# Kernel tuning notes

Measured on AMD Instinct MI355X. Metric: run time of the kernel, lower is better.

The kernel has to match this reference:

```python
import jax, jax.numpy as jnp
import numpy as np

N = 100000      # nodes
E = 1600000     # edges (avg degree 16)
D_IN, H, D_OUT = 128, 64, 40


def setup_inputs() -> dict:
    key = jax.random.key(0)
    k = jax.random.split(key, 6)
    x = jax.random.normal(k[0], (N, D_IN), dtype=jnp.float32)
    edge_index = jax.random.randint(k[1], (2, E), 0, N, dtype=jnp.int32)
    W1 = jax.random.normal(k[2], (D_IN, H), dtype=jnp.float32) / np.sqrt(D_IN)
    b1 = jnp.zeros((H,), dtype=jnp.float32)
    W2 = jax.random.normal(k[3], (H, D_OUT), dtype=jnp.float32) / np.sqrt(H)
    b2 = jnp.zeros((D_OUT,), dtype=jnp.float32)
    return {"x": x, "edge_index": edge_index, "W1": W1, "b1": b1, "W2": W2, "b2": b2}


def _gcn_conv(h, src, dst, dinv, W, b):
    # PyG GCNConv: linear transform, then D^-1/2 (A+I) D^-1/2 aggregation, then bias.
    h = h @ W                                   # [N, F]
    w = dinv[src] * dinv[dst]                   # [E] symmetric norm edge weights
    msg = h[src] * w[:, None]                   # [E, F] gather + scale
    agg = jax.ops.segment_sum(msg, dst, num_segments=N)  # scatter-add to dst
    agg = agg + h * (dinv * dinv)[:, None]      # self-loop contribution deg^-1 * h
    return agg + b


def reference(x, edge_index, W1, b1, W2, b2):
    src, dst = edge_index[0], edge_index[1]
    # degree with self-loops (in-degree at dst, source_to_target flow)
    deg = 1.0 + jax.ops.segment_sum(jnp.ones((E,), dtype=x.dtype), dst, num_segments=N)
    dinv = jax.lax.rsqrt(deg)
    # dropout (p=0.6) is identity in eval mode
    h = jax.nn.relu(_gcn_conv(x, src, dst, dinv, W1, b1))
    out = _gcn_conv(h, src, dst, dinv, W2, b2)
    return jax.nn.log_softmax(out, axis=1)
```

## Files before the change

### kernel.cpp

```cpp
#include <hip/hip_runtime.h>
#include <math.h>

#define D_IN  128
#define H_DIM 64
#define D_OUT 40
#define BW_SHIFT 9
#define BW_NODES 512
#define BINA_CHUNK 4096
#define BUCKET_CAP 9216

typedef unsigned int uint32;

__device__ __forceinline__ unsigned short f2bf(float v) {
    uint32 b = __float_as_uint(v);
    b += 0x7fffu + ((b >> 16) & 1u);
    return (unsigned short)(b >> 16);
}
__device__ __forceinline__ float bf2f(unsigned short u) {
    return __uint_as_float(((uint32)u) << 16);
}

__global__ void cursor_init_kernel(int* __restrict__ gcursor, int NBUCK) {
    int i = blockIdx.x * 256 + threadIdx.x;
    if (i < NBUCK) gcursor[i] = i * BUCKET_CAP;
}

__global__ __launch_bounds__(256) void binA_scatter_kernel(const int* __restrict__ src,
                                                           const int* __restrict__ dst,
                                                           int* __restrict__ gcursor,
                                                           uint32* __restrict__ binned,
                                                           int E, int NBUCK) {
    __shared__ int cnt[1024];
    __shared__ int lbase[1024];
    int t = threadIdx.x;
    for (int i = t; i < NBUCK; i += 256) cnt[i] = 0;
    __syncthreads();
    int e0 = blockIdx.x * BINA_CHUNK;
    int e1 = min(e0 + BINA_CHUNK, E);
    for (int e = e0 + t; e < e1; e += 256)
        atomicAdd(&cnt[dst[e] >> BW_SHIFT], 1);
    __syncthreads();
    for (int i = t; i < NBUCK; i += 256) {
        int c = cnt[i];
        lbase[i] = c ? atomicAdd(&gcursor[i], c) : 0;
        cnt[i] = 0;
    }
    __syncthreads();
    for (int e = e0 + t; e < e1; e += 256) {
        int d = dst[e];
        int bk = d >> BW_SHIFT;
        int p = lbase[bk] + atomicAdd(&cnt[bk], 1);
        binned[p] = (((uint32)(d & (BW_NODES - 1))) << 23) | (uint32)src[e];
    }
}

__global__ __launch_bounds__(256) void phaseB_kernel(uint32* __restrict__ binned,
                                                     const int* __restrict__ gcur_end,
                                                     int* __restrict__ rows,
                                                     float* __restrict__ dinv,
                                                     int N) {
    __shared__ uint32 sedge[BUCKET_CAP];
    __shared__ int deg[BW_NODES];
    __shared__ int sa[BW_NODES], sb[BW_NODES];
    __shared__ int cur[BW_NODES];
    int b = blockIdx.x;
    int node0 = b << BW_SHIFT;
    int nn = min(BW_NODES, N - node0);
    int base = b * BUCKET_CAP;
    int cnt = gcur_end[b] - base;
    int t = threadIdx.x;
    deg[t] = 0; deg[t + 256] = 0;
    __syncthreads();
    for (int e = t; e < cnt; e += 256) {
        uint32 v = binned[base + e];
        sedge[e] = v;
        atomicAdd(&deg[v >> 23], 1);
    }
    __syncthreads();
    for (int i = t; i < nn; i += 256)
        dinv[node0 + i] = rsqrtf(1.0f + (float)deg[i]);
    sa[t] = deg[t]; sa[t + 256] = deg[t + 256];
    __syncthreads();
    int* pa = sa; int* pb = sb;
    for (int off = 1; off < BW_NODES; off <<= 1) {
        for (int i = t; i < BW_NODES; i += 256)
            pb[i] = pa[i] + ((i >= off) ? pa[i - off] : 0);
        __syncthreads();
        int* tmp = pa; pa = pb; pb = tmp;
    }
    for (int i = t; i < BW_NODES; i += 256)
        cur[i] = (i ? pa[i - 1] : 0);
    __syncthreads();
    int* rb = rows + b * 513;
    for (int i = t; i < nn; i += 256)
        rb[i] = base + cur[i];
    if (t == 0) rb[nn] = base + cnt;
    __syncthreads();
    for (int e = t; e < cnt; e += 256) {
        uint32 v = sedge[e];
        int doff = v >> 23;
        int p = base + atomicAdd(&cur[doff], 1);
        binned[p] = v & 0x7FFFFFu;
    }
}

__global__ __launch_bounds__(256) void gemm1_tn4(const float* __restrict__ x,
                                                 const float* __restrict__ W1,
                                                 const float* __restrict__ dinv,
                                                 unsigned short* __restrict__ h1s, int N) {
    __shared__ float sW[D_IN * H_DIM];
    int t = threadIdx.x;
    for (int i = t; i < D_IN * H_DIM / 4; i += 256)
        reinterpret_cast<float4*>(sW)[i] = reinterpret_cast<const float4*>(W1)[i];
    __syncthreads();

    int n = blockIdx.x * 64 + (t >> 2);
    if (n >= N) return;
    int c0 = (t & 3) * 16;
    const float4* xr = reinterpret_cast<const float4*>(x + (size_t)n * D_IN);

    float acc[16] = {};
    for (int k0 = 0; k0 < D_IN / 4; ++k0) {
        float4 xv = xr[k0];
        #pragma unroll
        for (int kk = 0; kk < 4; ++kk) {
            float xk = (kk == 0) ? xv.x : (kk == 1) ? xv.y : (kk == 2) ? xv.z : xv.w;
            const float* wrow = &sW[(4 * k0 + kk) * H_DIM + c0];
            #pragma unroll
            for (int c = 0; c < 4; ++c) {
                float4 wv = *reinterpret_cast<const float4*>(wrow + 4 * c);
                acc[4 * c + 0] += xk * wv.x;
                acc[4 * c + 1] += xk * wv.y;
                acc[4 * c + 2] += xk * wv.z;
                acc[4 * c + 3] += xk * wv.w;
            }
        }
    }
    float di = dinv[n];
    unsigned short* orow = h1s + (size_t)n * H_DIM + c0;
    #pragma unroll
    for (int c = 0; c < 4; ++c) {
        ushort4 u;
        u.x = f2bf(acc[4 * c + 0] * di);
        u.y = f2bf(acc[4 * c + 1] * di);
        u.z = f2bf(acc[4 * c + 2] * di);
        u.w = f2bf(acc[4 * c + 3] * di);
        *reinterpret_cast<ushort4*>(orow + 4 * c) = u;
    }
}

__global__ __launch_bounds__(256) void agg1_v3(const int* __restrict__ rows,
                                               const int* __restrict__ csr,
                                               const unsigned short* __restrict__ h1s,
                                               const float* __restrict__ dinv,
                                               const float* __restrict__ b1,
                                               float* __restrict__ z, int N) {
    int node = blockIdx.x * 4 + (threadIdx.x >> 6);
    if (node >= N) return;
    int lane = threadIdx.x & 63;
    int e  = lane >> 4;
    int fl = (lane & 15) * 4;
    int ridx = node + (node >> BW_SHIFT);
    int s0 = __builtin_amdgcn_readfirstlane(rows[ridx]);
    int s1 = __builtin_amdgcn_readfirstlane(rows[ridx + 1]);

    float4 acc = make_float4(0.f, 0.f, 0.f, 0.f);
    for (int base = s0; base < s1; base += 64) {
        int cnt = min(64, s1 - base);
        int myc = (lane < cnt) ? csr[base + lane] : 0;
        int j = 0;
        for (; j + 8 <= cnt; j += 8) {
            uint32 sa = (uint32)__shfl(myc, j + e);
            uint32 sb = (uint32)__shfl(myc, j + 4 + e);
            ushort4 ha = *reinterpret_cast<const ushort4*>(h1s + (size_t)(sa * H_DIM + fl));
            ushort4 hb = *reinterpret_cast<const ushort4*>(h1s + (size_t)(sb * H_DIM + fl));
            acc.x += bf2f(ha.x) + bf2f(hb.x);
            acc.y += bf2f(ha.y) + bf2f(hb.y);
            acc.z += bf2f(ha.z) + bf2f(hb.z);
            acc.w += bf2f(ha.w) + bf2f(hb.w);
        }
        for (; j < cnt; j += 4) {
            int idx = j + e;
            uint32 sa = (uint32)__shfl(myc, min(idx, cnt - 1));
            if (idx < cnt) {
                ushort4 hv = *reinterpret_cast<const ushort4*>(h1s + (size_t)(sa * H_DIM + fl));
                acc.x += bf2f(hv.x); acc.y += bf2f(hv.y);
                acc.z += bf2f(hv.z); acc.w += bf2f(hv.w);
            }
        }
    }
    acc.x += __shfl_xor(acc.x, 16); acc.y += __shfl_xor(acc.y, 16);
    acc.z += __shfl_xor(acc.z, 16); acc.w += __shfl_xor(acc.w, 16);
    acc.x += __shfl_xor(acc.x, 32); acc.y += __shfl_xor(acc.y, 32);
    acc.z += __shfl_xor(acc.z, 32); acc.w += __shfl_xor(acc.w, 32);

    if (e == 0) {
        ushort4 sv = *reinterpret_cast<const ushort4*>(h1s + (size_t)node * H_DIM + fl);
        float4 bv = *reinterpret_cast<const float4*>(b1 + fl);
        float di = dinv[node];
        float4 o;
        o.x = fmaxf(0.f, di * (acc.x + bf2f(sv.x)) + bv.x);
        o.y = fmaxf(0.f, di * (acc.y + bf2f(sv.y)) + bv.y);
        o.z = fmaxf(0.f, di * (acc.z + bf2f(sv.z)) + bv.z);
        o.w = fmaxf(0.f, di * (acc.w + bf2f(sv.w)) + bv.w);
        *reinterpret_cast<float4*>(z + (size_t)node * H_DIM + fl) = o;
    }
}

__global__ __launch_bounds__(256) void gemm2_tn2(const float* __restrict__ z,
                                                 const float* __restrict__ W2,
                                                 const float* __restrict__ dinv,
                                                 unsigned short* __restrict__ h2s, int N) {
    __shared__ float sW[H_DIM * D_OUT];
    int t = threadIdx.x;
    for (int i = t; i < H_DIM * D_OUT / 4; i += 256)
        reinterpret_cast<float4*>(sW)[i] = reinterpret_cast<const float4*>(W2)[i];
    __syncthreads();

    int n = blockIdx.x * 128 + (t >> 1);
    if (n >= N) return;
    int c0 = (t & 1) * 20;
    const float4* zr = reinterpret_cast<const float4*>(z + (size_t)n * H_DIM);

    float acc[20] = {};
    for (int k0 = 0; k0 < H_DIM / 4; ++k0) {
        float4 zv = zr[k0];
        #pragma unroll
        for (int kk = 0; kk < 4; ++kk) {
            float zk = (kk == 0) ? zv.x : (kk == 1) ? zv.y : (kk == 2) ? zv.z : zv.w;
            const float* wrow = &sW[(4 * k0 + kk) * D_OUT + c0];
            #pragma unroll
            for (int c = 0; c < 5; ++c) {
                float4 wv = *reinterpret_cast<const float4*>(wrow + 4 * c);
                acc[4 * c + 0] += zk * wv.x;
                acc[4 * c + 1] += zk * wv.y;
                acc[4 * c + 2] += zk * wv.z;
                acc[4 * c + 3] += zk * wv.w;
            }
        }
    }
    float di = dinv[n];
    unsigned short* orow = h2s + (size_t)n * D_OUT + c0;
    #pragma unroll
    for (int c = 0; c < 5; ++c) {
        ushort4 u;
        u.x = f2bf(acc[4 * c + 0] * di);
        u.y = f2bf(acc[4 * c + 1] * di);
        u.z = f2bf(acc[4 * c + 2] * di);
        u.w = f2bf(acc[4 * c + 3] * di);
        *reinterpret_cast<ushort4*>(orow + 4 * c) = u;
    }
}

__global__ __launch_bounds__(256) void agg2_v4(const int* __restrict__ rows,
                                               const int* __restrict__ csr,
                                               const unsigned short* __restrict__ h2s,
                                               const float* __restrict__ dinv,
                                               const float* __restrict__ b2,
                                               float* __restrict__ out, int N) {
    int node = blockIdx.x * 4 + (threadIdx.x >> 6);
    if (node >= N) return;
    int lane = threadIdx.x & 63;
    int g   = lane / 10;
    int f10 = lane - g * 10;
    int fl  = f10 * 4;
    bool gact = g < 6;
    int ridx = node + (node >> BW_SHIFT);
    int s0 = __builtin_amdgcn_readfirstlane(rows[ridx]);
    int s1 = __builtin_amdgcn_readfirstlane(rows[ridx + 1]);

    float4 acc = make_float4(0.f, 0.f, 0.f, 0.f);
    for (int base = s0; base < s1; base += 64) {
        int cnt = min(64, s1 - base);
        int myc = (lane < cnt) ? csr[base + lane] : 0;
        int j = 0;
        for (; j + 12 <= cnt; j += 12) {
            uint32 sa = (uint32)__shfl(myc, min(j + g, 63));
            uint32 sb = (uint32)__shfl(myc, min(j + 6 + g, 63));
            if (gact) {
                ushort4 ha = *reinterpret_cast<const ushort4*>(h2s + (size_t)(sa * D_OUT + fl));
                ushort4 hb = *reinterpret_cast<const ushort4*>(h2s + (size_t)(sb * D_OUT + fl));
                acc.x += bf2f(ha.x) + bf2f(hb.x);
                acc.y += bf2f(ha.y) + bf2f(hb.y);
                acc.z += bf2f(ha.z) + bf2f(hb.z);
                acc.w += bf2f(ha.w) + bf2f(hb.w);
            }
        }
        for (; j < cnt; j += 6) {
            int idx = j + g;
            uint32 sa = (uint32)__shfl(myc, min(idx, cnt - 1));
            if (gact && idx < cnt) {
                ushort4 hv = *reinterpret_cast<const ushort4*>(h2s + (size_t)(sa * D_OUT + fl));
                acc.x += bf2f(hv.x); acc.y += bf2f(hv.y);
                acc.z += bf2f(hv.z); acc.w += bf2f(hv.w);
            }
        }
    }
    acc.x += __shfl(acc.x, min(lane + 30, 63));
    acc.y += __shfl(acc.y, min(lane + 30, 63));
    acc.z += __shfl(acc.z, min(lane + 30, 63));
    acc.w += __shfl(acc.w, min(lane + 30, 63));
    acc.x += __shfl(acc.x, min(lane + 10, 63)) + __shfl(acc.x, min(lane + 20, 63));
    acc.y += __shfl(acc.y, min(lane + 10, 63)) + __shfl(acc.y, min(lane + 20, 63));
    acc.z += __shfl(acc.z, min(lane + 10, 63)) + __shfl(acc.z, min(lane + 20, 63));
    acc.w += __shfl(acc.w, min(lane + 10, 63)) + __shfl(acc.w, min(lane + 20, 63));

    bool act = lane < 10;
    float v0 = -INFINITY, v1 = -INFINITY, v2 = -INFINITY, v3 = -INFINITY;
    if (act) {
        ushort4 sv = *reinterpret_cast<const ushort4*>(h2s + (size_t)node * D_OUT + fl);
        float4 bv = *reinterpret_cast<const float4*>(b2 + fl);
        float di = dinv[node];
        v0 = di * (acc.x + bf2f(sv.x)) + bv.x;
        v1 = di * (acc.y + bf2f(sv.y)) + bv.y;
        v2 = di * (acc.z + bf2f(sv.z)) + bv.z;
        v3 = di * (acc.w + bf2f(sv.w)) + bv.w;
    }
    float mm = act ? fmaxf(fmaxf(v0, v1), fmaxf(v2, v3)) : -INFINITY;
    for (int off = 32; off > 0; off >>= 1) mm = fmaxf(mm, __shfl_xor(mm, off));
    float es = act ? (__expf(v0 - mm) + __expf(v1 - mm) + __expf(v2 - mm) + __expf(v3 - mm)) : 0.f;
    for (int off = 32; off > 0; off >>= 1) es += __shfl_xor(es, off);
    float lse = __logf(es);
    if (act) {
        float4 o = make_float4(v0 - mm - lse, v1 - mm - lse, v2 - mm - lse, v3 - mm - lse);
        *reinterpret_cast<float4*>(out + (size_t)node * D_OUT + fl) = o;
    }
}

extern "C" void kernel_launch(void* const* d_in, const int* in_sizes, int n_in,
                              void* d_out, int out_size, void* d_ws, size_t ws_size,
                              hipStream_t stream) {
    const float* x  = (const float*)d_in[0];
    const int*   ei = (const int*)d_in[1];
    const float* W1 = (const float*)d_in[2];
    const float* b1 = (const float*)d_in[3];
    const float* W2 = (const float*)d_in[4];
    const float* b2 = (const float*)d_in[5];
    float* out = (float*)d_out;

    int N = in_sizes[0] / D_IN;
    int E = in_sizes[1] / 2;
    const int* src = ei;
    const int* dst = ei + E;
    int NBUCK = (N + BW_NODES - 1) / BW_NODES;

    char* p = (char*)d_ws;
    int*   gcursor = (int*)p;  p += 4096;
    int*   rows    = (int*)p;  p += ((size_t)NBUCK * 513 + 64) * 4;
    float* dinv    = (float*)p; p += (((size_t)N + 63) & ~(size_t)63) * 4;
    uint32* binned = (uint32*)p; p += (size_t)NBUCK * BUCKET_CAP * 4;
    unsigned short* h1s = (unsigned short*)p; p += (size_t)N * H_DIM * 2;
    float* z       = (float*)p; p += (size_t)N * H_DIM * 4;

    int binA_blocks = (E + BINA_CHUNK - 1) / BINA_CHUNK;

    cursor_init_kernel<<<(NBUCK + 255) / 256, 256, 0, stream>>>(gcursor, NBUCK);
    binA_scatter_kernel<<<binA_blocks, 256, 0, stream>>>(src, dst, gcursor, binned, E, NBUCK);
    phaseB_kernel<<<NBUCK, 256, 0, stream>>>(binned, gcursor, rows, dinv, N);
    int* csr = (int*)binned;

    gemm1_tn4<<<(N + 63) / 64, 256, 0, stream>>>(x, W1, dinv, h1s, N);
    agg1_v3<<<(N + 3) / 4, 256, 0, stream>>>(rows, csr, h1s, dinv, b1, z, N);

    unsigned short* h2s = h1s;
    gemm2_tn2<<<(N + 127) / 128, 256, 0, stream>>>(z, W2, dinv, h2s, N);
    agg2_v4<<<(N + 3) / 4, 256, 0, stream>>>(rows, csr, h2s, dinv, b2, out, N);
}
```

Measured before the change: 204.4 us.

## Fuse layer-1 aggregation with layer-2 GEMM in a persistent kernel

Merges the layer-1 aggregation and the layer-2 dense transform into one grid-stride kernel. Each wave aggregates a node, applies bias and ReLU, then computes the 40 outputs using shuffles and W2 held in shared memory, writing bf16 h2s directly. This removes the fp32 z intermediate round trip (write then read) and one kernel launch. Because h2s now gets its own buffer, it no longer aliases h1s. In exchange the per-node matvec is serialized within each wave, 24 of 64 lanes sit idle during it, and W2 is loaded into LDS once per block.

After: 252.1 us. 1.23x slower.

```diff
diff --git a/kernel.cpp b/kernel.cpp
--- a/kernel.cpp
+++ b/kernel.cpp
@@ -149,106 +149,81 @@
     }
 }
 
-__global__ __launch_bounds__(256) void agg1_v3(const int* __restrict__ rows,
-                                               const int* __restrict__ csr,
-                                               const unsigned short* __restrict__ h1s,
-                                               const float* __restrict__ dinv,
-                                               const float* __restrict__ b1,
-                                               float* __restrict__ z, int N) {
-    int node = blockIdx.x * 4 + (threadIdx.x >> 6);
-    if (node >= N) return;
-    int lane = threadIdx.x & 63;
+__global__ __launch_bounds__(256) void agg1g2_fused(const int* __restrict__ rows,
+                                                    const int* __restrict__ csr,
+                                                    const unsigned short* __restrict__ h1s,
+                                                    const float* __restrict__ dinv,
+                                                    const float* __restrict__ b1,
+                                                    const float* __restrict__ W2,
+                                                    unsigned short* __restrict__ h2s, int N) {
+    __shared__ float sW2[H_DIM * D_OUT];
+    int t = threadIdx.x;
+    for (int i = t; i < H_DIM * D_OUT / 4; i += 256)
+        reinterpret_cast<float4*>(sW2)[i] = reinterpret_cast<const float4*>(W2)[i];
+    __syncthreads();
+
+    int wid  = t >> 6;
+    int lane = t & 63;
     int e  = lane >> 4;
     int fl = (lane & 15) * 4;
-    int ridx = node + (node >> BW_SHIFT);
-    int s0 = __builtin_amdgcn_readfirstlane(rows[ridx]);
-    int s1 = __builtin_amdgcn_readfirstlane(rows[ridx + 1]);
-
-    float4 acc = make_float4(0.f, 0.f, 0.f, 0.f);
-    for (int base = s0; base < s1; base += 64) {
-        int cnt = min(64, s1 - base);
-        int myc = (lane < cnt) ? csr[base + lane] : 0;
-        int j = 0;
-        for (; j + 8 <= cnt; j += 8) {
-            uint32 sa = (uint32)__shfl(myc, j + e);
-            uint32 sb = (uint32)__shfl(myc, j + 4 + e);
-            ushort4 ha = *reinterpret_cast<const ushort4*>(h1s + (size_t)(sa * H_DIM + fl));
-            ushort4 hb = *reinterpret_cast<const ushort4*>(h1s + (size_t)(sb * H_DIM + fl));
-            acc.x += bf2f(ha.x) + bf2f(hb.x);
-            acc.y += bf2f(ha.y) + bf2f(hb.y);
-            acc.z += bf2f(ha.z) + bf2f(hb.z);
-            acc.w += bf2f(ha.w) + bf2f(hb.w);
-        }
-        for (; j < cnt; j += 4) {
-            int idx = j + e;
-            uint32 sa = (uint32)__shfl(myc, min(idx, cnt - 1));
-            if (idx < cnt) {
-                ushort4 hv = *reinterpret_cast<const ushort4*>(h1s + (size_t)(sa * H_DIM + fl));
-                acc.x += bf2f(hv.x); acc.y += bf2f(hv.y);
-                acc.z += bf2f(hv.z); acc.w += bf2f(hv.w);
-            }
-        }
-    }
-    acc.x += __shfl_xor(acc.x, 16); acc.y += __shfl_xor(acc.y, 16);
-    acc.z += __shfl_xor(acc.z, 16); acc.w += __shfl_xor(acc.w, 16);
-    acc.x += __shfl_xor(acc.x, 32); acc.y += __shfl_xor(acc.y, 32);
-    acc.z += __shfl_xor(acc.z, 32); acc.w += __shfl_xor(acc.w, 32);
-
-    if (e == 0) {
+    int lc = min(lane, D_OUT - 1);
+
+    for (int node = blockIdx.x * 4 + wid; node < N; node += gridDim.x * 4) {
+        int ridx = node + (node >> BW_SHIFT);
+        int s0 = __builtin_amdgcn_readfirstlane(rows[ridx]);
+        int s1 = __builtin_amdgcn_readfirstlane(rows[ridx + 1]);
+
+        float4 acc = make_float4(0.f, 0.f, 0.f, 0.f);
+        for (int base = s0; base < s1; base += 64) {
+            int cnt = min(64, s1 - base);
+            int myc = (lane < cnt) ? csr[base + lane] : 0;
+            int j = 0;
+            for (; j + 8 <= cnt; j += 8) {
+                uint32 sa = (uint32)__shfl(myc, j + e);
+                uint32 sb = (uint32)__shfl(myc, j + 4 + e);
+                ushort4 ha = *reinterpret_cast<const ushort4*>(h1s + (size_t)(sa * H_DIM + fl));
+                ushort4 hb = *reinterpret_cast<const ushort4*>(h1s + (size_t)(sb * H_DIM + fl));
+                acc.x += bf2f(ha.x) + bf2f(hb.x);
+                acc.y += bf2f(ha.y) + bf2f(hb.y);
+                acc.z += bf2f(ha.z) + bf2f(hb.z);
+                acc.w += bf2f(ha.w) + bf2f(hb.w);
+            }
+            for (; j < cnt; j += 4) {
+                int idx = j + e;
+                uint32 sa = (uint32)__shfl(myc, min(idx, cnt - 1));
+                if (idx < cnt) {
+                    ushort4 hv = *reinterpret_cast<const ushort4*>(h1s + (size_t)(sa * H_DIM + fl));
+                    acc.x += bf2f(hv.x); acc.y += bf2f(hv.y);
+                    acc.z += bf2f(hv.z); acc.w += bf2f(hv.w);
+                }
+            }
+        }
+        acc.x += __shfl_xor(acc.x, 16); acc.y += __shfl_xor(acc.y, 16);
+        acc.z += __shfl_xor(acc.z, 16); acc.w += __shfl_xor(acc.w, 16);
+        acc.x += __shfl_xor(acc.x, 32); acc.y += __shfl_xor(acc.y, 32);
+        acc.z += __shfl_xor(acc.z, 32); acc.w += __shfl_xor(acc.w, 32);
+
         ushort4 sv = *reinterpret_cast<const ushort4*>(h1s + (size_t)node * H_DIM + fl);
         float4 bv = *reinterpret_cast<const float4*>(b1 + fl);
         float di = dinv[node];
-        float4 o;
-        o.x = fmaxf(0.f, di * (acc.x + bf2f(sv.x)) + bv.x);
-        o.y = fmaxf(0.f, di * (acc.y + bf2f(sv.y)) + bv.y);
-        o.z = fmaxf(0.f, di * (acc.z + bf2f(sv.z)) + bv.z);
-        o.w = fmaxf(0.f, di * (acc.w + bf2f(sv.w)) + bv.w);
-        *reinterpret_cast<float4*>(z + (size_t)node * H_DIM + fl) = o;
-    }
-}
-
-__global__ __launch_bounds__(256) void gemm2_tn2(const float* __restrict__ z,
-                                                 const float* __restrict__ W2,
-                                                 const float* __restrict__ dinv,
-                                                 unsigned short* __restrict__ h2s, int N) {
-    __shared__ float sW[H_DIM * D_OUT];
-    int t = threadIdx.x;
-    for (int i = t; i < H_DIM * D_OUT / 4; i += 256)
-        reinterpret_cast<float4*>(sW)[i] = reinterpret_cast<const float4*>(W2)[i];
-    __syncthreads();
-
-    int n = blockIdx.x * 128 + (t >> 1);
-    if (n >= N) return;
-    int c0 = (t & 1) * 20;
-    const float4* zr = reinterpret_cast<const float4*>(z + (size_t)n * H_DIM);
-
-    float acc[20] = {};
-    for (int k0 = 0; k0 < H_DIM / 4; ++k0) {
-        float4 zv = zr[k0];
+        float4 z4;
+        z4.x = fmaxf(0.f, di * (acc.x + bf2f(sv.x)) + bv.x);
+        z4.y = fmaxf(0.f, di * (acc.y + bf2f(sv.y)) + bv.y);
+        z4.z = fmaxf(0.f, di * (acc.z + bf2f(sv.z)) + bv.z);
+        z4.w = fmaxf(0.f, di * (acc.w + bf2f(sv.w)) + bv.w);
+
+        float acc2 = 0.f;
         #pragma unroll
-        for (int kk = 0; kk < 4; ++kk) {
-            float zk = (kk == 0) ? zv.x : (kk == 1) ? zv.y : (kk == 2) ? zv.z : zv.w;
-            const float* wrow = &sW[(4 * k0 + kk) * D_OUT + c0];
-            #pragma unroll
-            for (int c = 0; c < 5; ++c) {
-                float4 wv = *reinterpret_cast<const float4*>(wrow + 4 * c);
-                acc[4 * c + 0] += zk * wv.x;
-                acc[4 * c + 1] += zk * wv.y;
-                acc[4 * c + 2] += zk * wv.z;
-                acc[4 * c + 3] += zk * wv.w;
-            }
-        }
-    }
-    float di = dinv[n];
-    unsigned short* orow = h2s + (size_t)n * D_OUT + c0;
-    #pragma unroll
-    for (int c = 0; c < 5; ++c) {
-        ushort4 u;
-        u.x = f2bf(acc[4 * c + 0] * di);
-        u.y = f2bf(acc[4 * c + 1] * di);
-        u.z = f2bf(acc[4 * c + 2] * di);
-        u.w = f2bf(acc[4 * c + 3] * di);
-        *reinterpret_cast<ushort4*>(orow + 4 * c) = u;
+        for (int k0 = 0; k0 < H_DIM / 4; ++k0) {
+            float zx = __shfl(z4.x, k0);
+            float zy = __shfl(z4.y, k0);
+            float zz = __shfl(z4.z, k0);
+            float zw = __shfl(z4.w, k0);
+            const float* wr = &sW2[4 * k0 * D_OUT + lc];
+            acc2 += zx * wr[0] + zy * wr[D_OUT] + zz * wr[2 * D_OUT] + zw * wr[3 * D_OUT];
+        }
+        if (lane < D_OUT)
+            h2s[(size_t)node * D_OUT + lane] = f2bf(acc2 * di);
     }
 }
 
@@ -350,7 +325,7 @@
     float* dinv    = (float*)p; p += (((size_t)N + 63) & ~(size_t)63) * 4;
     uint32* binned = (uint32*)p; p += (size_t)NBUCK * BUCKET_CAP * 4;
     unsigned short* h1s = (unsigned short*)p; p += (size_t)N * H_DIM * 2;
-    float* z       = (float*)p; p += (size_t)N * H_DIM * 4;
+    unsigned short* h2s = (unsigned short*)p; p += (((size_t)N * D_OUT * 2 + 255) & ~(size_t)255);
 
     int binA_blocks = (E + BINA_CHUNK - 1) / BINA_CHUNK;
 
@@ -360,9 +335,9 @@
     int* csr = (int*)binned;
 
     gemm1_tn4<<<(N + 63) / 64, 256, 0, stream>>>(x, W1, dinv, h1s, N);
-    agg1_v3<<<(N + 3) / 4, 256, 0, stream>>>(rows, csr, h1s, dinv, b1, z, N);
-
-    unsigned short* h2s = h1s;
-    gemm2_tn2<<<(N + 127) / 128, 256, 0, stream>>>(z, W2, dinv, h2s, N);
+
+    int fgrid = min((N + 3) / 4, 4096);
+    agg1g2_fused<<<fgrid, 256, 0, stream>>>(rows, csr, h1s, dinv, b1, W2, h2s, N);
+
     agg2_v4<<<(N + 3) / 4, 256, 0, stream>>>(rows, csr, h2s, dinv, b2, out, N);
 }
```

## Split feature matrices into column panels and aggregate panel-by-panel for cache locality

Applied to the files above, without the earlier changes.

The bf16 transformed features are now stored panel-major: layer 1 uses 4 panels of 16 columns and layer 2 uses 2 panels of 20 columns. The aggregation kernels run one pass per panel, launching more blocks, so each pass gathers from a smaller working set that is more likely to stay in L2/MALL. The cost is re-reading CSR indices and row pointers once per panel. Because a layer-2 pass sees only half the columns, log_softmax moves into a separate kernel, which adds an extra read and write of the output.

Result: slower. 307.3 us (+50.3%).

```diff
diff --git a/kernel.cpp b/kernel.cpp
--- a/kernel.cpp
+++ b/kernel.cpp
@@ -107,7 +107,7 @@
 __global__ __launch_bounds__(256) void gemm1_tn4(const float* __restrict__ x,
                                                  const float* __restrict__ W1,
                                                  const float* __restrict__ dinv,
-                                                 unsigned short* __restrict__ h1s, int N) {
+                                                 unsigned short* __restrict__ h1t, int N) {
     __shared__ float sW[D_IN * H_DIM];
     int t = threadIdx.x;
     for (int i = t; i < D_IN * H_DIM / 4; i += 256)
@@ -116,7 +116,8 @@
 
     int n = blockIdx.x * 64 + (t >> 2);
     if (n >= N) return;
-    int c0 = (t & 3) * 16;
+    int p  = t & 3;
+    int c0 = p * 16;
     const float4* xr = reinterpret_cast<const float4*>(x + (size_t)n * D_IN);
 
     float acc[16] = {};
@@ -137,7 +138,7 @@
         }
     }
     float di = dinv[n];
-    unsigned short* orow = h1s + (size_t)n * H_DIM + c0;
+    unsigned short* orow = h1t + ((size_t)p * N + n) * 16;
     #pragma unroll
     for (int c = 0; c < 4; ++c) {
         ushort4 u;
@@ -149,68 +150,71 @@
     }
 }
 
-__global__ __launch_bounds__(256) void agg1_v3(const int* __restrict__ rows,
-                                               const int* __restrict__ csr,
-                                               const unsigned short* __restrict__ h1s,
-                                               const float* __restrict__ dinv,
-                                               const float* __restrict__ b1,
-                                               float* __restrict__ z, int N) {
-    int node = blockIdx.x * 4 + (threadIdx.x >> 6);
+__global__ __launch_bounds__(256) void agg1_pass(const int* __restrict__ rows,
+                                                 const int* __restrict__ csr,
+                                                 const unsigned short* __restrict__ h1t,
+                                                 const float* __restrict__ dinv,
+                                                 const float* __restrict__ b1,
+                                                 float* __restrict__ z, int N, int NB) {
+    int bid = blockIdx.x;
+    int p = bid / NB;
+    int node = (bid - p * NB) * 4 + (threadIdx.x >> 6);
     if (node >= N) return;
     int lane = threadIdx.x & 63;
-    int e  = lane >> 4;
-    int fl = (lane & 15) * 4;
+    int e  = lane >> 2;
+    int fo = (lane & 3) * 4;
+    size_t pN = (size_t)p * N;
     int ridx = node + (node >> BW_SHIFT);
     int s0 = __builtin_amdgcn_readfirstlane(rows[ridx]);
     int s1 = __builtin_amdgcn_readfirstlane(rows[ridx + 1]);
 
-    float4 acc = make_float4(0.f, 0.f, 0.f, 0.f);
+    float a0 = 0.f, a1 = 0.f, a2 = 0.f, a3 = 0.f;
     for (int base = s0; base < s1; base += 64) {
         int cnt = min(64, s1 - base);
         int myc = (lane < cnt) ? csr[base + lane] : 0;
         int j = 0;
-        for (; j + 8 <= cnt; j += 8) {
+        for (; j + 16 <= cnt; j += 16) {
             uint32 sa = (uint32)__shfl(myc, j + e);
-            uint32 sb = (uint32)__shfl(myc, j + 4 + e);
-            ushort4 ha = *reinterpret_cast<const ushort4*>(h1s + (size_t)(sa * H_DIM + fl));
-            ushort4 hb = *reinterpret_cast<const ushort4*>(h1s + (size_t)(sb * H_DIM + fl));
-            acc.x += bf2f(ha.x) + bf2f(hb.x);
-            acc.y += bf2f(ha.y) + bf2f(hb.y);
-            acc.z += bf2f(ha.z) + bf2f(hb.z);
-            acc.w += bf2f(ha.w) + bf2f(hb.w);
-        }
-        for (; j < cnt; j += 4) {
+            uint2 hv = *reinterpret_cast<const uint2*>(h1t + (pN + sa) * 16 + fo);
+            a0 += __uint_as_float(hv.x << 16);
+            a1 += __uint_as_float(hv.x & 0xffff0000u);
+            a2 += __uint_as_float(hv.y << 16);
+            a3 += __uint_as_float(hv.y & 0xffff0000u);
+        }
+        if (j < cnt) {
             int idx = j + e;
             uint32 sa = (uint32)__shfl(myc, min(idx, cnt - 1));
             if (idx < cnt) {
-                ushort4 hv = *reinterpret_cast<const ushort4*>(h1s + (size_t)(sa * H_DIM + fl));
-                acc.x += bf2f(hv.x); acc.y += bf2f(hv.y);
-                acc.z += bf2f(hv.z); acc.w += bf2f(hv.w);
-            }
-        }
-    }
-    acc.x += __shfl_xor(acc.x, 16); acc.y += __shfl_xor(acc.y, 16);
-    acc.z += __shfl_xor(acc.z, 16); acc.w += __shfl_xor(acc.w, 16);
-    acc.x += __shfl_xor(acc.x, 32); acc.y += __shfl_xor(acc.y, 32);
-    acc.z += __shfl_xor(acc.z, 32); acc.w += __shfl_xor(acc.w, 32);
+                uint2 hv = *reinterpret_cast<const uint2*>(h1t + (pN + sa) * 16 + fo);
+                a0 += __uint_as_float(hv.x << 16);
+                a1 += __uint_as_float(hv.x & 0xffff0000u);
+                a2 += __uint_as_float(hv.y << 16);
+                a3 += __uint_as_float(hv.y & 0xffff0000u);
+            }
+        }
+    }
+    a0 += __shfl_xor(a0, 4);  a1 += __shfl_xor(a1, 4);  a2 += __shfl_xor(a2, 4);  a3 += __shfl_xor(a3, 4);
+    a0 += __shfl_xor(a0, 8);  a1 += __shfl_xor(a1, 8);  a2 += __shfl_xor(a2, 8);  a3 += __shfl_xor(a3, 8);
+    a0 += __shfl_xor(a0, 16); a1 += __shfl_xor(a1, 16); a2 += __shfl_xor(a2, 16); a3 += __shfl_xor(a3, 16);
+    a0 += __shfl_xor(a0, 32); a1 += __shfl_xor(a1, 32); a2 += __shfl_xor(a2, 32); a3 += __shfl_xor(a3, 32);
 
     if (e == 0) {
-        ushort4 sv = *reinterpret_cast<const ushort4*>(h1s + (size_t)node * H_DIM + fl);
-        float4 bv = *reinterpret_cast<const float4*>(b1 + fl);
+        uint2 sv = *reinterpret_cast<const uint2*>(h1t + (pN + node) * 16 + fo);
+        float4 bv = *reinterpret_cast<const float4*>(b1 + p * 16 + fo);
         float di = dinv[node];
         float4 o;
-        o.x = fmaxf(0.f, di * (acc.x + bf2f(sv.x)) + bv.x);
-        o.y = fmaxf(0.f, di * (acc.y + bf2f(sv.y)) + bv.y);
-        o.z = fmaxf(0.f, di * (acc.z + bf2f(sv.z)) + bv.z);
-        o.w = fmaxf(0.f, di * (acc.w + bf2f(sv.w)) + bv.w);
-        *reinterpret_cast<float4*>(z + (size_t)node * H_DIM + fl) = o;
+        o.x = fmaxf(0.f, di * (a0 + __uint_as_float(sv.x << 16)) + bv.x);
+        o.y = fmaxf(0.f, di * (a1 + __uint_as_float(sv.x & 0xffff0000u)) + bv.y);
+        o.z = fmaxf(0.f, di * (a2 + __uint_as_float(sv.y << 16)) + bv.z);
+        o.w = fmaxf(0.f, di * (a3 + __uint_as_float(sv.y & 0xffff0000u)) + bv.w);
+        *reinterpret_cast<float4*>(z + (size_t)node * H_DIM + p * 16 + fo) = o;
     }
 }
 
 __global__ __launch_bounds__(256) void gemm2_tn2(const float* __restrict__ z,
                                                  const float* __restrict__ W2,
                                                  const float* __restrict__ dinv,
-                                                 unsigned short* __restrict__ h2s, int N) {
+                                                 unsigned short* __restrict__ h2t, int N) {
     __shared__ float sW[H_DIM * D_OUT];
     int t = threadIdx.x;
     for (int i = t; i < H_DIM * D_OUT / 4; i += 256)
@@ -219,7 +223,8 @@
 
     int n = blockIdx.x * 128 + (t >> 1);
     if (n >= N) return;
-    int c0 = (t & 1) * 20;
+    int q  = t & 1;
+    int c0 = q * 20;
     const float4* zr = reinterpret_cast<const float4*>(z + (size_t)n * H_DIM);
 
     float acc[20] = {};
@@ -240,7 +245,7 @@
         }
     }
     float di = dinv[n];
-    unsigned short* orow = h2s + (size_t)n * D_OUT + c0;
+    unsigned short* orow = h2t + ((size_t)q * N + n) * 20;
     #pragma unroll
     for (int c = 0; c < 5; ++c) {
         ushort4 u;
@@ -252,79 +257,87 @@
     }
 }
 
-__global__ __launch_bounds__(256) void agg2_v4(const int* __restrict__ rows,
-                                               const int* __restrict__ csr,
-                                               const unsigned short* __restrict__ h2s,
-                                               const float* __restrict__ dinv,
-                                               const float* __restrict__ b2,
-                                               float* __restrict__ out, int N) {
-    int node = blockIdx.x * 4 + (threadIdx.x >> 6);
+__global__ __launch_bounds__(256) void agg2_pass(const int* __restrict__ rows,
+                                                 const int* __restrict__ csr,
+                                                 const unsigned short* __restrict__ h2t,
+                                                 const float* __restrict__ dinv,
+                                                 const float* __restrict__ b2,
+                                                 float* __restrict__ out, int N, int NB) {
+    int bid = blockIdx.x;
+    int q = bid / NB;
+    int node = (bid - q * NB) * 4 + (threadIdx.x >> 6);
     if (node >= N) return;
     int lane = threadIdx.x & 63;
-    int g   = lane / 10;
-    int f10 = lane - g * 10;
-    int fl  = f10 * 4;
-    bool gact = g < 6;
+    int g  = lane / 5;
+    int fo = (lane - g * 5) * 4;
+    bool gact = g < 12;
+    size_t qN = (size_t)q * N;
     int ridx = node + (node >> BW_SHIFT);
     int s0 = __builtin_amdgcn_readfirstlane(rows[ridx]);
     int s1 = __builtin_amdgcn_readfirstlane(rows[ridx + 1]);
 
-    float4 acc = make_float4(0.f, 0.f, 0.f, 0.f);
+    float a0 = 0.f, a1 = 0.f, a2 = 0.f, a3 = 0.f;
     for (int base = s0; base < s1; base += 64) {
         int cnt = min(64, s1 - base);
         int myc = (lane < cnt) ? csr[base + lane] : 0;
         int j = 0;
         for (; j + 12 <= cnt; j += 12) {
-            uint32 sa = (uint32)__shfl(myc, min(j + g, 63));
-            uint32 sb = (uint32)__shfl(myc, min(j + 6 + g, 63));
+            uint32 sa = (uint32)__shfl(myc, min(j + g, cnt - 1));
             if (gact) {
-                ushort4 ha = *reinterpret_cast<const ushort4*>(h2s + (size_t)(sa * D_OUT + fl));
-                ushort4 hb = *reinterpret_cast<const ushort4*>(h2s + (size_t)(sb * D_OUT + fl));
-                acc.x += bf2f(ha.x) + bf2f(hb.x);
-                acc.y += bf2f(ha.y) + bf2f(hb.y);
-                acc.z += bf2f(ha.z) + bf2f(hb.z);
-                acc.w += bf2f(ha.w) + bf2f(hb.w);
-            }
-        }
-        for (; j < cnt; j += 6) {
+                uint2 hv = *reinterpret_cast<const uint2*>(h2t + (qN + sa) * 20 + fo);
+                a0 += __uint_as_float(hv.x << 16);
+                a1 += __uint_as_float(hv.x & 0xffff0000u);
+                a2 += __uint_as_float(hv.y << 16);
+                a3 += __uint_as_float(hv.y & 0xffff0000u);
+            }
+        }
+        if (j < cnt) {
             int idx = j + g;
             uint32 sa = (uint32)__shfl(myc, min(idx, cnt - 1));
             if (gact && idx < cnt) {
-                ushort4 hv = *reinterpret_cast<const ushort4*>(h2s + (size_t)(sa * D_OUT + fl));
-                acc.x += bf2f(hv.x); acc.y += bf2f(hv.y);
-                acc.z += bf2f(hv.z); acc.w += bf2f(hv.w);
-            }
-        }
-    }
-    acc.x += __shfl(acc.x, min(lane + 30, 63));
-    acc.y += __shfl(acc.y, min(lane + 30, 63));
-    acc.z += __shfl(acc.z, min(lane + 30, 63));
-    acc.w += __shfl(acc.w, min(lane + 30, 63));
-    acc.x += __shfl(acc.x, min(lane + 10, 63)) + __shfl(acc.x, min(lane + 20, 63));
-    acc.y += __shfl(acc.y, min(lane + 10, 63)) + __shfl(acc.y, min(lane + 20, 63));
-    acc.z += __shfl(acc.z, min(lane + 10, 63)) + __shfl(acc.z, min(lane + 20, 63));
-    acc.w += __shfl(acc.w, min(lane + 10, 63)) + __shfl(acc.w, min(lane + 20, 63));
-
-    bool act = lane < 10;
-    float v0 = -INFINITY, v1 = -INFINITY, v2 = -INFINITY, v3 = -INFINITY;
-    if (act) {
-        ushort4 sv = *reinterpret_cast<const ushort4*>(h2s + (size_t)node * D_OUT + fl);
-        float4 bv = *reinterpret_cast<const float4*>(b2 + fl);
+                uint2 hv = *reinterpret_cast<const uint2*>(h2t + (qN + sa) * 20 + fo);
+                a0 += __uint_as_float(hv.x << 16);
+                a1 += __uint_as_float(hv.x & 0xffff0000u);
+                a2 += __uint_as_float(hv.y << 16);
+                a3 += __uint_as_float(hv.y & 0xffff0000u);
+            }
+        }
+    }
+    a0 += __shfl(a0, min(lane + 30, 63)); a1 += __shfl(a1, min(lane + 30, 63));
+    a2 += __shfl(a2, min(lane + 30, 63)); a3 += __shfl(a3, min(lane + 30, 63));
+    a0 += __shfl(a0, min(lane + 15, 63)); a1 += __shfl(a1, min(lane + 15, 63));
+    a2 += __shfl(a2, min(lane + 15, 63)); a3 += __shfl(a3, min(lane + 15, 63));
+    a0 += __shfl(a0, min(lane + 5, 63)) + __shfl(a0, min(lane + 10, 63));
+    a1 += __shfl(a1, min(lane + 5, 63)) + __shfl(a1, min(lane + 10, 63));
+    a2 += __shfl(a2, min(lane + 5, 63)) + __shfl(a2, min(lane + 10, 63));
+    a3 += __shfl(a3, min(lane + 5, 63)) + __shfl(a3, min(lane + 10, 63));
+
+    if (lane < 5) {
+        uint2 sv = *reinterpret_cast<const uint2*>(h2t + (qN + node) * 20 + fo);
+        float4 bv = *reinterpret_cast<const float4*>(b2 + q * 20 + fo);
         float di = dinv[node];
-        v0 = di * (acc.x + bf2f(sv.x)) + bv.x;
-        v1 = di * (acc.y + bf2f(sv.y)) + bv.y;
-        v2 = di * (acc.z + bf2f(sv.z)) + bv.z;
-        v3 = di * (acc.w + bf2f(sv.w)) + bv.w;
-    }
-    float mm = act ? fmaxf(fmaxf(v0, v1), fmaxf(v2, v3)) : -INFINITY;
-    for (int off = 32; off > 0; off >>= 1) mm = fmaxf(mm, __shfl_xor(mm, off));
-    float es = act ? (__expf(v0 - mm) + __expf(v1 - mm) + __expf(v2 - mm) + __expf(v3 - mm)) : 0.f;
-    for (int off = 32; off > 0; off >>= 1) es += __shfl_xor(es, off);
-    float lse = __logf(es);
-    if (act) {
-        float4 o = make_float4(v0 - mm - lse, v1 - mm - lse, v2 - mm - lse, v3 - mm - lse);
-        *reinterpret_cast<float4*>(out + (size_t)node * D_OUT + fl) = o;
-    }
+        float4 o;
+        o.x = di * (a0 + __uint_as_float(sv.x << 16)) + bv.x;
+        o.y = di * (a1 + __uint_as_float(sv.x & 0xffff0000u)) + bv.y;
+        o.z = di * (a2 + __uint_as_float(sv.y << 16)) + bv.z;
+        o.w = di * (a3 + __uint_as_float(sv.y & 0xffff0000u)) + bv.w;
+        *reinterpret_cast<float4*>(out + (size_t)node * D_OUT + q * 20 + fo) = o;
+    }
+}
+
+__global__ __launch_bounds__(256) void softmax_kernel(float* __restrict__ out, int N) {
+    int node = blockIdx.x * 4 + (threadIdx.x >> 6);
+    if (node >= N) return;
+    int lane = threadIdx.x & 63;
+    float v = (lane < D_OUT) ? out[(size_t)node * D_OUT + lane] : -INFINITY;
+    float m = v;
+    for (int off = 32; off > 0; off >>= 1) m = fmaxf(m, __shfl_xor(m, off));
+    float ex = (lane < D_OUT) ? __expf(v - m) : 0.f;
+    float s = ex;
+    for (int off = 32; off > 0; off >>= 1) s += __shfl_xor(s, off);
+    float lse = __logf(s);
+    if (lane < D_OUT)
+        out[(size_t)node * D_OUT + lane] = v - m - lse;
 }
 
 extern "C" void kernel_launch(void* const* d_in, const int* in_sizes, int n_in,
@@ -349,20 +362,22 @@
     int*   rows    = (int*)p;  p += ((size_t)NBUCK * 513 + 64) * 4;
     float* dinv    = (float*)p; p += (((size_t)N + 63) & ~(size_t)63) * 4;
     uint32* binned = (uint32*)p; p += (size_t)NBUCK * BUCKET_CAP * 4;
-    unsigned short* h1s = (unsigned short*)p; p += (size_t)N * H_DIM * 2;
+    unsigned short* h1t = (unsigned short*)p; p += (size_t)N * H_DIM * 2;
+    unsigned short* h2t = (unsigned short*)p; p += (((size_t)N * D_OUT * 2 + 255) & ~(size_t)255);
     float* z       = (float*)p; p += (size_t)N * H_DIM * 4;
 
     int binA_blocks = (E + BINA_CHUNK - 1) / BINA_CHUNK;
+    int NB = (N + 3) / 4;
 
     cursor_init_kernel<<<(NBUCK + 255) / 256, 256, 0, stream>>>(gcursor, NBUCK);
     binA_scatter_kernel<<<binA_blocks, 256, 0, stream>>>(src, dst, gcursor, binned, E, NBUCK);
     phaseB_kernel<<<NBUCK, 256, 0, stream>>>(binned, gcursor, rows, dinv, N);
     int* csr = (int*)binned;
 
-    gemm1_tn4<<<(N + 63) / 64, 256, 0, stream>>>(x, W1, dinv, h1s, N);
-    agg1_v3<<<(N + 3) / 4, 256, 0, stream>>>(rows, csr, h1s, dinv, b1, z, N);
-
-    unsigned short* h2s = h1s;
-    gemm2_tn2<<<(N + 127) / 128, 256, 0, stream>>>(z, W2, dinv, h2s, N);
-    agg2_v4<<<(N + 3) / 4, 256, 0, stream>>>(rows, csr, h2s, dinv, b2, out, N);
-}
+    gemm1_tn4<<<(N + 63) / 64, 256, 0, stream>>>(x, W1, dinv, h1t, N);
+    agg1_pass<<<4 * NB, 256, 0, stream>>>(rows, csr, h1t, dinv, b1, z, N, NB);
+
+    gemm2_tn2<<<(N + 127) / 128, 256, 0, stream>>>(z, W2, dinv, h2t, N);
+    agg2_pass<<<2 * NB, 256, 0, stream>>>(rows, csr, h2t, dinv, b2, out, N, NB);
+    softmax_kernel<<<NB, 256, 0, stream>>>(out, N);
+}
```

## Fuse edge binning with first GEMM and apply dinv scaling in phase B

Applied to the files above, without the earlier changes.

The edge-binning scatter and the first dense transform x@W1 now run as one launch, with block ranges split between the two jobs, so the GEMM no longer waits for the degree computation. Because dinv is not yet known during the GEMM, h1 is stored unscaled in bf16 and phaseB rescales each row by dinv after computing the degrees. This removes a launch and overlaps the compute-bound GEMM with the atomic-heavy binning. In exchange it adds an extra read-modify-write pass over h1 in phaseB and rounds to bf16 twice, which changes precision slightly.

After: 208.8 us. +2.2%, slower.

```diff
diff --git a/kernel.cpp b/kernel.cpp
--- a/kernel.cpp
+++ b/kernel.cpp
@@ -25,96 +25,49 @@
     if (i < NBUCK) gcursor[i] = i * BUCKET_CAP;
 }
 
-__global__ __launch_bounds__(256) void binA_scatter_kernel(const int* __restrict__ src,
-                                                           const int* __restrict__ dst,
-                                                           int* __restrict__ gcursor,
-                                                           uint32* __restrict__ binned,
-                                                           int E, int NBUCK) {
-    __shared__ int cnt[1024];
-    __shared__ int lbase[1024];
+__global__ __launch_bounds__(256) void binA_gemm1_fused(const int* __restrict__ src,
+                                                        const int* __restrict__ dst,
+                                                        int* __restrict__ gcursor,
+                                                        uint32* __restrict__ binned,
+                                                        int E, int NBUCK, int binA_blocks,
+                                                        const float* __restrict__ x,
+                                                        const float* __restrict__ W1,
+                                                        unsigned short* __restrict__ h1s, int N) {
+    __shared__ float smem[D_IN * H_DIM];
     int t = threadIdx.x;
-    for (int i = t; i < NBUCK; i += 256) cnt[i] = 0;
-    __syncthreads();
-    int e0 = blockIdx.x * BINA_CHUNK;
-    int e1 = min(e0 + BINA_CHUNK, E);
-    for (int e = e0 + t; e < e1; e += 256)
-        atomicAdd(&cnt[dst[e] >> BW_SHIFT], 1);
-    __syncthreads();
-    for (int i = t; i < NBUCK; i += 256) {
-        int c = cnt[i];
-        lbase[i] = c ? atomicAdd(&gcursor[i], c) : 0;
-        cnt[i] = 0;
-    }
-    __syncthreads();
-    for (int e = e0 + t; e < e1; e += 256) {
-        int d = dst[e];
-        int bk = d >> BW_SHIFT;
-        int p = lbase[bk] + atomicAdd(&cnt[bk], 1);
-        binned[p] = (((uint32)(d & (BW_NODES - 1))) << 23) | (uint32)src[e];
-    }
-}
-
-__global__ __launch_bounds__(256) void phaseB_kernel(uint32* __restrict__ binned,
-                                                     const int* __restrict__ gcur_end,
-                                                     int* __restrict__ rows,
-                                                     float* __restrict__ dinv,
-                                                     int N) {
-    __shared__ uint32 sedge[BUCKET_CAP];
-    __shared__ int deg[BW_NODES];
-    __shared__ int sa[BW_NODES], sb[BW_NODES];
-    __shared__ int cur[BW_NODES];
-    int b = blockIdx.x;
-    int node0 = b << BW_SHIFT;
-    int nn = min(BW_NODES, N - node0);
-    int base = b * BUCKET_CAP;
-    int cnt = gcur_end[b] - base;
-    int t = threadIdx.x;
-    deg[t] = 0; deg[t + 256] = 0;
-    __syncthreads();
-    for (int e = t; e < cnt; e += 256) {
-        uint32 v = binned[base + e];
-        sedge[e] = v;
-        atomicAdd(&deg[v >> 23], 1);
-    }
-    __syncthreads();
-    for (int i = t; i < nn; i += 256)
-        dinv[node0 + i] = rsqrtf(1.0f + (float)deg[i]);
-    sa[t] = deg[t]; sa[t + 256] = deg[t + 256];
-    __syncthreads();
-    int* pa = sa; int* pb = sb;
-    for (int off = 1; off < BW_NODES; off <<= 1) {
-        for (int i = t; i < BW_NODES; i += 256)
-            pb[i] = pa[i] + ((i >= off) ? pa[i - off] : 0);
+
+    if (blockIdx.x < binA_blocks) {
+        int* cnt   = (int*)smem;
+        int* lbase = cnt + 1024;
+        for (int i = t; i < NBUCK; i += 256) cnt[i] = 0;
         __syncthreads();
-        int* tmp = pa; pa = pb; pb = tmp;
-    }
-    for (int i = t; i < BW_NODES; i += 256)
-        cur[i] = (i ? pa[i - 1] : 0);
-    __syncthreads();
-    int* rb = rows + b * 513;
-    for (int i = t; i < nn; i += 256)
-        rb[i] = base + cur[i];
-    if (t == 0) rb[nn] = base + cnt;
-    __syncthreads();
-    for (int e = t; e < cnt; e += 256) {
-        uint32 v = sedge[e];
-        int doff = v >> 23;
-        int p = base + atomicAdd(&cur[doff], 1);
-        binned[p] = v & 0x7FFFFFu;
-    }
-}
-
-__global__ __launch_bounds__(256) void gemm1_tn4(const float* __restrict__ x,
-                                                 const float* __restrict__ W1,
-                                                 const float* __restrict__ dinv,
-                                                 unsigned short* __restrict__ h1s, int N) {
-    __shared__ float sW[D_IN * H_DIM];
-    int t = threadIdx.x;
+        int e0 = blockIdx.x * BINA_CHUNK;
+        int e1 = min(e0 + BINA_CHUNK, E);
+        for (int e = e0 + t; e < e1; e += 256)
+            atomicAdd(&cnt[dst[e] >> BW_SHIFT], 1);
+        __syncthreads();
+        for (int i = t; i < NBUCK; i += 256) {
+            int c = cnt[i];
+            lbase[i] = c ? atomicAdd(&gcursor[i], c) : 0;
+            cnt[i] = 0;
+        }
+        __syncthreads();
+        for (int e = e0 + t; e < e1; e += 256) {
+            int d = dst[e];
+            int bk = d >> BW_SHIFT;
+            int p = lbase[bk] + atomicAdd(&cnt[bk], 1);
+            binned[p] = (((uint32)(d & (BW_NODES - 1))) << 23) | (uint32)src[e];
+        }
+        return;
+    }
+
+    float* sW = smem;
     for (int i = t; i < D_IN * H_DIM / 4; i += 256)
         reinterpret_cast<float4*>(sW)[i] = reinterpret_cast<const float4*>(W1)[i];
     __syncthreads();
 
-    int n = blockIdx.x * 64 + (t >> 2);
+    int gb = blockIdx.x - binA_blocks;
+    int n = gb * 64 + (t >> 2);
     if (n >= N) return;
     int c0 = (t & 3) * 16;
     const float4* xr = reinterpret_cast<const float4*>(x + (size_t)n * D_IN);
@@ -136,16 +89,82 @@
             }
         }
     }
-    float di = dinv[n];
     unsigned short* orow = h1s + (size_t)n * H_DIM + c0;
     #pragma unroll
     for (int c = 0; c < 4; ++c) {
         ushort4 u;
-        u.x = f2bf(acc[4 * c + 0] * di);
-        u.y = f2bf(acc[4 * c + 1] * di);
-        u.z = f2bf(acc[4 * c + 2] * di);
-        u.w = f2bf(acc[4 * c + 3] * di);
+        u.x = f2bf(acc[4 * c + 0]);
+        u.y = f2bf(acc[4 * c + 1]);
+        u.z = f2bf(acc[4 * c + 2]);
+        u.w = f2bf(acc[4 * c + 3]);
         *reinterpret_cast<ushort4*>(orow + 4 * c) = u;
+    }
+}
+
+__global__ __launch_bounds__(256) void phaseB_kernel(uint32* __restrict__ binned,
+                                                     const int* __restrict__ gcur_end,
+                                                     int* __restrict__ rows,
+                                                     float* __restrict__ dinv,
+                                                     unsigned short* __restrict__ h1s,
+                                                     int N) {
+    __shared__ uint32 sedge[BUCKET_CAP];
+    __shared__ int deg[BW_NODES];
+    __shared__ int sa[BW_NODES], sb[BW_NODES];
+    __shared__ int cur[BW_NODES];
+    __shared__ float sdinv[BW_NODES];
+    int b = blockIdx.x;
+    int node0 = b << BW_SHIFT;
+    int nn = min(BW_NODES, N - node0);
+    int base = b * BUCKET_CAP;
+    int cnt = gcur_end[b] - base;
+    int t = threadIdx.x;
+    deg[t] = 0; deg[t + 256] = 0;
+    __syncthreads();
+    for (int e = t; e < cnt; e += 256) {
+        uint32 v = binned[base + e];
+        sedge[e] = v;
+        atomicAdd(&deg[v >> 23], 1);
+    }
+    __syncthreads();
+    for (int i = t; i < nn; i += 256) {
+        float di = rsqrtf(1.0f + (float)deg[i]);
+        sdinv[i] = di;
+        dinv[node0 + i] = di;
+    }
+    sa[t] = deg[t]; sa[t + 256] = deg[t + 256];
+    __syncthreads();
+    int* pa = sa; int* pb = sb;
+    for (int off = 1; off < BW_NODES; off <<= 1) {
+        for (int i = t; i < BW_NODES; i += 256)
+            pb[i] = pa[i] + ((i >= off) ? pa[i - off] : 0);
+        __syncthreads();
+        int* tmp = pa; pa = pb; pb = tmp;
+    }
+    for (int i = t; i < BW_NODES; i += 256)
+        cur[i] = (i ? pa[i - 1] : 0);
+    __syncthreads();
+    int* rb = rows + b * 513;
+    for (int i = t; i < nn; i += 256)
+        rb[i] = base + cur[i];
+    if (t == 0) rb[nn] = base + cnt;
+    __syncthreads();
+    for (int e = t; e < cnt; e += 256) {
+        uint32 v = sedge[e];
+        int doff = v >> 23;
+        int p = base + atomicAdd(&cur[doff], 1);
+        binned[p] = v & 0x7FFFFFu;
+    }
+    for (int i = t; i < nn * 16; i += 256) {
+        int n  = i >> 4;
+        int c4 = (i & 15) * 4;
+        float di = sdinv[n];
+        unsigned short* row = h1s + (size_t)(node0 + n) * H_DIM + c4;
+        ushort4 u = *reinterpret_cast<ushort4*>(row);
+        u.x = f2bf(bf2f(u.x) * di);
+        u.y = f2bf(bf2f(u.y) * di);
+        u.z = f2bf(bf2f(u.z) * di);
+        u.w = f2bf(bf2f(u.w) * di);
+        *reinterpret_cast<ushort4*>(row) = u;
     }
 }
 
@@ -352,14 +371,15 @@
     unsigned short* h1s = (unsigned short*)p; p += (size_t)N * H_DIM * 2;
     float* z       = (float*)p; p += (size_t)N * H_DIM * 4;
 
-    int binA_blocks = (E + BINA_CHUNK - 1) / BINA_CHUNK;
+    int binA_blocks  = (E + BINA_CHUNK - 1) / BINA_CHUNK;
+    int gemm1_blocks = (N + 63) / 64;
 
     cursor_init_kernel<<<(NBUCK + 255) / 256, 256, 0, stream>>>(gcursor, NBUCK);
-    binA_scatter_kernel<<<binA_blocks, 256, 0, stream>>>(src, dst, gcursor, binned, E, NBUCK);
-    phaseB_kernel<<<NBUCK, 256, 0, stream>>>(binned, gcursor, rows, dinv, N);
+    binA_gemm1_fused<<<binA_blocks + gemm1_blocks, 256, 0, stream>>>(
+        src, dst, gcursor, binned, E, NBUCK, binA_blocks, x, W1, h1s, N);
+    phaseB_kernel<<<NBUCK, 256, 0, stream>>>(binned, gcursor, rows, dinv, h1s, N);
     int* csr = (int*)binned;
 
-    gemm1_tn4<<<(N + 63) / 64, 256, 0, stream>>>(x, W1, dinv, h1s, N);
     agg1_v3<<<(N + 3) / 4, 256, 0, stream>>>(rows, csr, h1s, dinv, b1, z, N);
 
     unsigned short* h2s = h1s;
```
